# Performance work log

Hardware: AMD Instinct MI355X
Metric: run time of the kernel (lower is better)

## Reference

```python
import jax, jax.numpy as jnp
import numpy as np

N, E = 50000, 800000
IN_DIM, HID, HEADS, LAYERS = 128, 128, 4, 2
C = HID // HEADS  # per-head channels
LN_EPS = 1e-5


def _segment_softmax(logits, seg, num_segments):
    # logits: [E, H], seg: [E] target-node ids
    m = jax.ops.segment_max(logits, seg, num_segments=num_segments)  # [N, H]
    ex = jnp.exp(logits - m[seg])
    s = jax.ops.segment_sum(ex, seg, num_segments=num_segments)      # [N, H]
    return ex / s[seg]


def setup_inputs() -> dict:
    key = jax.random.key(0)
    ks = jax.random.split(key, 16)
    x = jax.random.normal(ks[0], (N, IN_DIM), dtype=jnp.float32)
    edge_index = jax.random.randint(ks[1], (2, E), 0, N, dtype=jnp.int64)
    edge_weight = jax.random.normal(ks[2], (E,), dtype=jnp.float32)
    s = 0.05
    # stacked per-layer params (in_ch == hidden for both layers since in_dim == hidden_dim)
    Wq = jax.random.normal(ks[3], (LAYERS, HID, HID), dtype=jnp.float32) * s
    bq = jnp.zeros((LAYERS, HID), dtype=jnp.float32)
    Wk = jax.random.normal(ks[4], (LAYERS, HID, HID), dtype=jnp.float32) * s
    bk = jnp.zeros((LAYERS, HID), dtype=jnp.float32)
    Wv = jax.random.normal(ks[5], (LAYERS, HID, HID), dtype=jnp.float32) * s
    bv = jnp.zeros((LAYERS, HID), dtype=jnp.float32)
    We = jax.random.normal(ks[6], (LAYERS, 1, HID), dtype=jnp.float32) * s  # lin_edge, no bias
    Wskip = jax.random.normal(ks[7], (LAYERS, HID, HID), dtype=jnp.float32) * s
    bskip = jnp.zeros((LAYERS, HID), dtype=jnp.float32)
    ln_g = jnp.ones((LAYERS, HID), dtype=jnp.float32)
    ln_b = jnp.zeros((LAYERS, HID), dtype=jnp.float32)
    return dict(x=x, edge_index=edge_index, edge_weight=edge_weight,
                Wq=Wq, bq=bq, Wk=Wk, bk=bk, Wv=Wv, bv=bv, We=We,
                Wskip=Wskip, bskip=bskip, ln_g=ln_g, ln_b=ln_b)


def reference(x, edge_index, edge_weight, Wq, bq, Wk, bk, Wv, bv, We, Wskip, bskip, ln_g, ln_b):
    # eval mode: dropout (on alpha and on features) is identity
    h = jnp.nan_to_num(x, nan=0.0, posinf=0.0, neginf=0.0)
    edge_attr = jnp.nan_to_num(edge_weight, nan=0.0, posinf=0.0, neginf=0.0)[:, None]  # [E,1]
    src, dst = edge_index[0], edge_index[1]  # PyG: x_j = x[src], softmax/aggregate over dst
    scale = 1.0 / jnp.sqrt(jnp.asarray(C, dtype=h.dtype))
    for l in range(LAYERS):
        h_res = h
        q = (h @ Wq[l] + bq[l]).reshape(N, HEADS, C)
        k = (h @ Wk[l] + bk[l]).reshape(N, HEADS, C)
        v = (h @ Wv[l] + bv[l]).reshape(N, HEADS, C)
        e = (edge_attr @ We[l]).reshape(E, HEADS, C)          # lin_edge (bias=False)
        kj = k[src] + e                                       # [E,H,C]
        logits = jnp.einsum('ehc,ehc->eh', q[dst], kj) * scale
        alpha = _segment_softmax(logits, dst, N)              # [E,H]
        msg = (v[src] + e) * alpha[..., None]                 # [E,H,C]
        out = jax.ops.segment_sum(msg, dst, num_segments=N).reshape(N, HID)
        out = out + h @ Wskip[l] + bskip[l]                   # root_weight skip (beta=False)
        out = jnp.nan_to_num(out, nan=0.0, posinf=0.0, neginf=0.0)
        mu = out.mean(axis=-1, keepdims=True)
        var = ((out - mu) ** 2).mean(axis=-1, keepdims=True)
        out = (out - mu) / jnp.sqrt(var + LN_EPS) * ln_g[l] + ln_b[l]
        out = jax.nn.relu(jnp.nan_to_num(out, nan=0.0, posinf=0.0, neginf=0.0))
        out = jnp.nan_to_num(out, nan=0.0, posinf=0.0, neginf=0.0)
        h = jnp.nan_to_num(out + h_res, nan=0.0, posinf=0.0, neginf=0.0)
    return h
```

## Files before the change

### kernel.cpp

```cpp
#include <hip/hip_runtime.h>
#include <hip/hip_fp16.h>
#include <math.h>

#define NN 50000
#define EE 800000
#define HID 128
#define LAYERS 2
#define LN_EPS 1e-5f
#define SCALE 0.17677669529663687f
#define NB 49

typedef _Float16 f16x8 __attribute__((ext_vector_type(8)));
typedef _Float16 h2 __attribute__((ext_vector_type(2)));
typedef float f32x4 __attribute__((ext_vector_type(4)));

__device__ __forceinline__ float sanitize(float f) {
    return (f == f && fabsf(f) != INFINITY) ? f : 0.0f;
}


__global__ void zero_deg_kernel(int* __restrict__ deg) {
    int i = blockIdx.x * blockDim.x + threadIdx.x;
    if (i < NN) deg[i] = 0;
}

__global__ void hist_kernel(const int* __restrict__ eidx, int* __restrict__ deg) {
    int e = blockIdx.x * blockDim.x + threadIdx.x;
    if (e < EE) atomicAdd(&deg[eidx[EE + e]], 1);
}


__global__ __launch_bounds__(1024) void deg_bsum_kernel(const int* __restrict__ deg,
                                                        int* __restrict__ bsum) {
    __shared__ int red[16];
    int tid = threadIdx.x;
    int i = blockIdx.x * 1024 + tid;
    int v = (i < NN) ? deg[i] : 0;
    #pragma unroll
    for (int off = 32; off >= 1; off >>= 1) v += __shfl_xor(v, off, 64);
    if ((tid & 63) == 0) red[tid >> 6] = v;
    __syncthreads();
    if (tid == 0) {
        int s = 0;
        #pragma unroll
        for (int w = 0; w < 16; ++w) s += red[w];
        bsum[blockIdx.x] = s;
    }
}

__global__ void bsum_scan_kernel(const int* __restrict__ bsum, int* __restrict__ boff,
                                 int* __restrict__ row_start) {
    int lane = threadIdx.x;
    int v = (lane < NB) ? bsum[lane] : 0;
    int sc = v;
    #pragma unroll
    for (int off = 1; off < 64; off <<= 1) {
        int t = __shfl_up(sc, off, 64);
        if (lane >= off) sc += t;
    }
    if (lane < NB) boff[lane] = sc - v;
    if (lane == 63) row_start[NN] = sc;
}

__global__ __launch_bounds__(1024) void deg_scan_kernel(const int* __restrict__ deg,
                                                        const int* __restrict__ boff,
                                                        int* __restrict__ row_start,
                                                        int* __restrict__ cursor) {
    __shared__ int wsum[16];
    int tid = threadIdx.x;
    int lane = tid & 63;
    int wid = tid >> 6;
    int i = blockIdx.x * 1024 + tid;
    int val = (i < NN) ? deg[i] : 0;
    int sc = val;
    #pragma unroll
    for (int off = 1; off < 64; off <<= 1) {
        int t = __shfl_up(sc, off, 64);
        if (lane >= off) sc += t;
    }
    if (lane == 63) wsum[wid] = sc;
    __syncthreads();
    if (wid == 0) {
        int s = (lane < 16) ? wsum[lane] : 0;
        #pragma unroll
        for (int off = 1; off < 16; off <<= 1) {
            int t = __shfl_up(s, off, 64);
            if (lane >= off) s += t;
        }
        if (lane < 16) wsum[lane] = s;
    }
    __syncthreads();
    int waveoff = (wid > 0) ? wsum[wid - 1] : 0;
    int excl = boff[blockIdx.x] + waveoff + sc - val;
    if (i < NN) {
        row_start[i] = excl;
        cursor[i] = excl;
    }
}

__global__ void scatter_kernel(const int* __restrict__ eidx,
                               const float* __restrict__ ew,
                               int* __restrict__ cursor,
                               long long* __restrict__ csr_pk) {
    int e = blockIdx.x * blockDim.x + threadIdx.x;
    if (e < EE) {
        int dst = eidx[EE + e];
        int src = eidx[e];
        int pos = atomicAdd(&cursor[dst], 1);
        unsigned wb = __float_as_uint(sanitize(ew[e]));
        csr_pk[pos] = ((long long)wb << 32) | (unsigned)src;
    }
}


__global__ void sanitize_kernel(const float* __restrict__ x, float* __restrict__ h0,
                                __half* __restrict__ hh) {
    int i = blockIdx.x * blockDim.x + threadIdx.x;
    if (i < NN * HID / 4) {
        float4 f = ((const float4*)x)[i];
        f.x = sanitize(f.x); f.y = sanitize(f.y); f.z = sanitize(f.z); f.w = sanitize(f.w);
        ((float4*)h0)[i] = f;
        __half2* hp = (__half2*)(hh + (size_t)i * 4);
        hp[0] = __floats2half2_rn(f.x, f.y);
        hp[1] = __floats2half2_rn(f.z, f.w);
    }
}


__global__ void wtcvt_kernel(const float* __restrict__ Wq, const float* __restrict__ Wk,
                             const float* __restrict__ Wv, const float* __restrict__ Wsk,
                             __half* __restrict__ WT) {
    int idx = blockIdx.x * blockDim.x + threadIdx.x;
    if (idx >= LAYERS * 4 * HID * HID) return;
    int k = idx & 127;
    int c = (idx >> 7) & 127;
    int m = (idx >> 14) & 3;
    int l = idx >> 16;
    const float* W = (m == 0) ? Wq : (m == 1) ? Wk : (m == 2) ? Wv : Wsk;
    WT[idx] = __float2half(W[l * HID * HID + k * HID + c]);
}


__global__ __launch_bounds__(256) void mfma_qkvs_kernel(
    const __half* __restrict__ hh, const __half* __restrict__ WT,
    const float* __restrict__ bq, const float* __restrict__ bk,
    const float* __restrict__ bv, const float* __restrict__ bsk,
    __half* __restrict__ qh, __half* __restrict__ kv, float* __restrict__ skf)
{
    int wid = threadIdx.x >> 6;
    int lane = threadIdx.x & 63;
    int row0 = blockIdx.x * 64 + wid * 16;
    int arow = row0 + (lane & 15);
    if (arow >= NN) arow = NN - 1;
    int ksub = (lane >> 4) * 8;

    const _Float16* hp = (const _Float16*)(hh + (size_t)arow * HID + ksub);
    f16x8 a0 = *(const f16x8*)(hp + 0);
    f16x8 a1 = *(const f16x8*)(hp + 32);
    f16x8 a2 = *(const f16x8*)(hp + 64);
    f16x8 a3 = *(const f16x8*)(hp + 96);

    #pragma unroll
    for (int m = 0; m < 4; ++m) {
        const _Float16* Wm = (const _Float16*)(WT + m * HID * HID);
        const float* bias = (m == 0) ? bq : (m == 1) ? bk : (m == 2) ? bv : bsk;
        #pragma unroll
        for (int t = 0; t < 8; ++t) {
            int col = t * 16 + (lane & 15);
            const _Float16* wc = Wm + (size_t)col * HID + ksub;
            f32x4 acc = {0.f, 0.f, 0.f, 0.f};
            acc = __builtin_amdgcn_mfma_f32_16x16x32_f16(a0, *(const f16x8*)(wc + 0),  acc, 0, 0, 0);
            acc = __builtin_amdgcn_mfma_f32_16x16x32_f16(a1, *(const f16x8*)(wc + 32), acc, 0, 0, 0);
            acc = __builtin_amdgcn_mfma_f32_16x16x32_f16(a2, *(const f16x8*)(wc + 64), acc, 0, 0, 0);
            acc = __builtin_amdgcn_mfma_f32_16x16x32_f16(a3, *(const f16x8*)(wc + 96), acc, 0, 0, 0);
            float bcol = bias[col];
            #pragma unroll
            for (int r = 0; r < 4; ++r) {
                int row = row0 + (lane >> 4) * 4 + r;
                if (row < NN) {
                    float val = acc[r] + bcol;
                    if (m == 0)      qh[(size_t)row * HID + col] = __float2half(val);
                    else if (m == 1) kv[(size_t)row * 256 + col] = __float2half(val);
                    else if (m == 2) kv[(size_t)row * 256 + 128 + col] = __float2half(val);
                    else             skf[(size_t)row * HID + col] = val;
                }
            }
        }
    }
}


struct OS8 { float m, s, tw; float a[8]; };

__device__ __forceinline__ void os8_init(OS8& o) {
    o.m = -INFINITY; o.s = 0.f; o.tw = 0.f;
    #pragma unroll
    for (int j = 0; j < 8; ++j) o.a[j] = 0.f;
}

__device__ __forceinline__ OS8 os8_mrg(OS8 a, OS8 b) {
    float mn = fmaxf(a.m, b.m);
    if (mn == -INFINITY) return a;
    float ca = __expf(a.m - mn);
    float cb = __expf(b.m - mn);
    OS8 r;
    r.m = mn;
    r.s  = a.s  * ca + b.s  * cb;
    r.tw = a.tw * ca + b.tw * cb;
    #pragma unroll
    for (int j = 0; j < 8; ++j) r.a[j] = a.a[j] * ca + b.a[j] * cb;
    return r;
}

__device__ __forceinline__ void edge_step(long long p, const __half* __restrict__ kv, int c0,
                                          h2 q01, h2 q23, h2 q45, h2 q67, float qwe, OS8& st) {
    int src = (int)(p & 0xffffffffLL);
    float w = __uint_as_float((unsigned)((unsigned long long)p >> 32));
    const _Float16* kvp = (const _Float16*)(kv + (size_t)src * 256);
    f16x8 k8 = *(const f16x8*)(kvp + c0);
    f16x8 v8 = *(const f16x8*)(kvp + 128 + c0);
    h2 k01 = {k8[0], k8[1]}, k23 = {k8[2], k8[3]}, k45 = {k8[4], k8[5]}, k67 = {k8[6], k8[7]};
    float d = __builtin_amdgcn_fdot2(k01, q01, 0.f, false);
    d = __builtin_amdgcn_fdot2(k23, q23, d, false);
    d = __builtin_amdgcn_fdot2(k45, q45, d, false);
    d = __builtin_amdgcn_fdot2(k67, q67, d, false);
    d += __shfl_xor(d, 1, 64);
    d += __shfl_xor(d, 2, 64);
    float l = fmaf(w, qwe, d) * SCALE;
    float mn = fmaxf(st.m, l);
    float cr = __expf(st.m - mn);
    float pp = __expf(l - mn);
    st.s  = fmaf(st.s,  cr, pp);
    st.tw = fmaf(st.tw, cr, pp * w);
    #pragma unroll
    for (int j = 0; j < 8; ++j) st.a[j] = fmaf(st.a[j], cr, pp * (float)v8[j]);
    st.m = mn;
}

__global__ __launch_bounds__(256) void agg_kernel(
    const __half* __restrict__ qh, const __half* __restrict__ kv,
    const float* __restrict__ skp, const float* __restrict__ hres,
    const float* __restrict__ We,
    const float* __restrict__ ln_g, const float* __restrict__ ln_b,
    const int* __restrict__ row_start, const long long* __restrict__ csr_pk,
    float* __restrict__ hout, __half* __restrict__ hh_out)
{
    int node = blockIdx.x * 16 + (threadIdx.x >> 4);
    int sl = threadIdx.x & 15;
    int c0 = sl * 8;

    f16x8 q8 = *(const f16x8*)((const _Float16*)qh + (size_t)node * HID + c0);
    h2 q01 = {q8[0], q8[1]}, q23 = {q8[2], q8[3]}, q45 = {q8[4], q8[5]}, q67 = {q8[6], q8[7]};

    float4 weA = *(const float4*)(We + c0);
    float4 weB = *(const float4*)(We + c0 + 4);
    float qwe = (float)q8[0] * weA.x + (float)q8[1] * weA.y + (float)q8[2] * weA.z + (float)q8[3] * weA.w
              + (float)q8[4] * weB.x + (float)q8[5] * weB.y + (float)q8[6] * weB.z + (float)q8[7] * weB.w;
    qwe += __shfl_xor(qwe, 1, 64);
    qwe += __shfl_xor(qwe, 2, 64);

    int rs = row_start[node];
    int re = row_start[node + 1];

    OS8 st0, st1, st2, st3;
    os8_init(st0); os8_init(st1); os8_init(st2); os8_init(st3);

    int i = rs;
    for (; i + 4 <= re; i += 4) {
        long long p0 = csr_pk[i + 0];
        long long p1 = csr_pk[i + 1];
        long long p2 = csr_pk[i + 2];
        long long p3 = csr_pk[i + 3];
        edge_step(p0, kv, c0, q01, q23, q45, q67, qwe, st0);
        edge_step(p1, kv, c0, q01, q23, q45, q67, qwe, st1);
        edge_step(p2, kv, c0, q01, q23, q45, q67, qwe, st2);
        edge_step(p3, kv, c0, q01, q23, q45, q67, qwe, st3);
    }
    for (; i < re; ++i) edge_step(csr_pk[i], kv, c0, q01, q23, q45, q67, qwe, st0);

    OS8 st = os8_mrg(os8_mrg(st0, st1), os8_mrg(st2, st3));

    float inv = (re > rs) ? 1.f / st.s : 0.f;
    float wef[8] = {weA.x, weA.y, weA.z, weA.w, weB.x, weB.y, weB.z, weB.w};

    float4 skA = *(const float4*)(skp + (size_t)node * HID + c0);
    float4 skB = *(const float4*)(skp + (size_t)node * HID + c0 + 4);
    float skv[8] = {skA.x, skA.y, skA.z, skA.w, skB.x, skB.y, skB.z, skB.w};

    float ox[8];
    float sum8 = 0.f;
    #pragma unroll
    for (int j = 0; j < 8; ++j) {
        float o = fmaf(st.tw, wef[j], st.a[j]) * inv;
        o = sanitize(o + skv[j]);
        ox[j] = o;
        sum8 += o;
    }

    float mu = sum8;
    mu += __shfl_xor(mu, 1, 64); mu += __shfl_xor(mu, 2, 64);
    mu += __shfl_xor(mu, 4, 64); mu += __shfl_xor(mu, 8, 64);
    mu *= (1.f / 128.f);

    float var8 = 0.f;
    #pragma unroll
    for (int j = 0; j < 8; ++j) {
        float dx = ox[j] - mu;
        var8 = fmaf(dx, dx, var8);
    }
    float var = var8;
    var += __shfl_xor(var, 1, 64); var += __shfl_xor(var, 2, 64);
    var += __shfl_xor(var, 4, 64); var += __shfl_xor(var, 8, 64);
    var *= (1.f / 128.f);
    float rstd = rsqrtf(var + LN_EPS);

    float4 gA = *(const float4*)(ln_g + c0);
    float4 gB = *(const float4*)(ln_g + c0 + 4);
    float4 bA = *(const float4*)(ln_b + c0);
    float4 bB = *(const float4*)(ln_b + c0 + 4);
    float gv[8] = {gA.x, gA.y, gA.z, gA.w, gB.x, gB.y, gB.z, gB.w};
    float bv_[8] = {bA.x, bA.y, bA.z, bA.w, bB.x, bB.y, bB.z, bB.w};

    float4 hrA = *(const float4*)(hres + (size_t)node * HID + c0);
    float4 hrB = *(const float4*)(hres + (size_t)node * HID + c0 + 4);
    float hr[8] = {hrA.x, hrA.y, hrA.z, hrA.w, hrB.x, hrB.y, hrB.z, hrB.w};

    float outv[8];
    _Float16 outh[8];
    #pragma unroll
    for (int j = 0; j < 8; ++j) {
        float rx = fmaxf(fmaf((ox[j] - mu) * rstd, gv[j], bv_[j]), 0.f);
        float o = sanitize(rx + hr[j]);
        outv[j] = o;
        outh[j] = (_Float16)o;
    }
    float* op = hout + (size_t)node * HID + c0;
    *(float4*)(op)     = make_float4(outv[0], outv[1], outv[2], outv[3]);
    *(float4*)(op + 4) = make_float4(outv[4], outv[5], outv[6], outv[7]);
    *(f16x8*)((_Float16*)hh_out + (size_t)node * HID + c0) =
        *(f16x8*)outh;
}


extern "C" void kernel_launch(void* const* d_in, const int* in_sizes, int n_in,
                              void* d_out, int out_size, void* d_ws, size_t ws_size,
                              hipStream_t stream) {
    const float* x      = (const float*)d_in[0];
    const int*   ei     = (const int*)d_in[1];
    const float* ew     = (const float*)d_in[2];
    const float* Wq     = (const float*)d_in[3];
    const float* bq     = (const float*)d_in[4];
    const float* Wk     = (const float*)d_in[5];
    const float* bk     = (const float*)d_in[6];
    const float* Wv     = (const float*)d_in[7];
    const float* bv     = (const float*)d_in[8];
    const float* We     = (const float*)d_in[9];
    const float* Wsk    = (const float*)d_in[10];
    const float* bsk    = (const float*)d_in[11];
    const float* ln_g   = (const float*)d_in[12];
    const float* ln_b   = (const float*)d_in[13];

    const size_t NH = (size_t)NN * HID;
    float* h0  = (float*)d_ws;
    float* h1  = h0 + NH;
    float* skf = h1 + NH;
    __half* hh = (__half*)(skf + NH);
    __half* qh = hh + NH;
    __half* kv = qh + NH;
    __half* WT = kv + 2 * NH;
    int* deg       = (int*)(WT + LAYERS * 4 * HID * HID);
    int* row_start = deg + NN;
    int* cursor    = row_start + NN + 2;
    int* bsum      = cursor + NN;
    int* boff      = bsum + 64;
    long long* csr_pk = (long long*)(boff + 64);

    zero_deg_kernel<<<(NN + 255) / 256, 256, 0, stream>>>(deg);
    hist_kernel<<<(EE + 255) / 256, 256, 0, stream>>>(ei, deg);
    deg_bsum_kernel<<<NB, 1024, 0, stream>>>(deg, bsum);
    bsum_scan_kernel<<<1, 64, 0, stream>>>(bsum, boff, row_start);
    deg_scan_kernel<<<NB, 1024, 0, stream>>>(deg, boff, row_start, cursor);
    scatter_kernel<<<(EE + 255) / 256, 256, 0, stream>>>(ei, ew, cursor, csr_pk);

    sanitize_kernel<<<(NN * HID / 4 + 255) / 256, 256, 0, stream>>>(x, h0, hh);
    wtcvt_kernel<<<(LAYERS * 4 * HID * HID + 255) / 256, 256, 0, stream>>>(Wq, Wk, Wv, Wsk, WT);

    const int WELEM = HID * HID;
    const int MROWS = (NN + 63) / 64;

    for (int l = 0; l < LAYERS; ++l) {
        const float* hin = (l == 0) ? h0 : h1;
        float* hout = (l == 0) ? h1 : (float*)d_out;
        mfma_qkvs_kernel<<<MROWS, 256, 0, stream>>>(
            hh, WT + (size_t)l * 4 * WELEM,
            bq + l * HID, bk + l * HID, bv + l * HID, bsk + l * HID,
            qh, kv, skf);
        agg_kernel<<<NN / 16, 256, 0, stream>>>(
            qh, kv, skf, hin,
            We + l * HID, ln_g + l * HID, ln_b + l * HID,
            row_start, csr_pk, hout, hh);
    }
}
```

Before: 472.8 us.

## Assign one wavefront per node and split edges across four lane groups

The aggregation kernel now maps each destination node to a full 64-lane wavefront instead of a 16-lane group. The four 16-lane groups each process an interleaved subset of the node's edges with two online-softmax states, then merge them through cross-group shuffles. The goal is more memory-level parallelism per node and shorter serial edge chains, since mean degree is 16. The cost is four times as many blocks, redundant epilogue work on three quarters of the lanes, and extra shuffle traffic for the merge.

```diff
diff --git a/kernel.cpp b/kernel.cpp
--- a/kernel.cpp
+++ b/kernel.cpp
@@ -212,6 +212,16 @@
     return r;
 }
 
+__device__ __forceinline__ OS8 os8_shfl_xor(const OS8& o, int mask) {
+    OS8 r;
+    r.m  = __shfl_xor(o.m,  mask, 64);
+    r.s  = __shfl_xor(o.s,  mask, 64);
+    r.tw = __shfl_xor(o.tw, mask, 64);
+    #pragma unroll
+    for (int j = 0; j < 8; ++j) r.a[j] = __shfl_xor(o.a[j], mask, 64);
+    return r;
+}
+
 __device__ __forceinline__ void edge_step(long long p, const __half* __restrict__ kv, int c0,
                                           h2 q01, h2 q23, h2 q45, h2 q67, float qwe, OS8& st) {
     int src = (int)(p & 0xffffffffLL);
@@ -245,8 +255,10 @@
     const int* __restrict__ row_start, const long long* __restrict__ csr_pk,
     float* __restrict__ hout, __half* __restrict__ hh_out)
 {
-    int node = blockIdx.x * 16 + (threadIdx.x >> 4);
-    int sl = threadIdx.x & 15;
+    int node = blockIdx.x * 4 + (threadIdx.x >> 6);
+    int lane = threadIdx.x & 63;
+    int grp = lane >> 4;
+    int sl = lane & 15;
     int c0 = sl * 8;
 
     f16x8 q8 = *(const f16x8*)((const _Float16*)qh + (size_t)node * HID + c0);
@@ -262,23 +274,21 @@
     int rs = row_start[node];
     int re = row_start[node + 1];
 
-    OS8 st0, st1, st2, st3;
-    os8_init(st0); os8_init(st1); os8_init(st2); os8_init(st3);
-
-    int i = rs;
-    for (; i + 4 <= re; i += 4) {
-        long long p0 = csr_pk[i + 0];
-        long long p1 = csr_pk[i + 1];
-        long long p2 = csr_pk[i + 2];
-        long long p3 = csr_pk[i + 3];
-        edge_step(p0, kv, c0, q01, q23, q45, q67, qwe, st0);
-        edge_step(p1, kv, c0, q01, q23, q45, q67, qwe, st1);
-        edge_step(p2, kv, c0, q01, q23, q45, q67, qwe, st2);
-        edge_step(p3, kv, c0, q01, q23, q45, q67, qwe, st3);
-    }
-    for (; i < re; ++i) edge_step(csr_pk[i], kv, c0, q01, q23, q45, q67, qwe, st0);
-
-    OS8 st = os8_mrg(os8_mrg(st0, st1), os8_mrg(st2, st3));
+    OS8 s0, s1;
+    os8_init(s0); os8_init(s1);
+
+    int i = rs + grp;
+    for (; i + 4 < re; i += 8) {
+        long long p0 = csr_pk[i];
+        long long p1 = csr_pk[i + 4];
+        edge_step(p0, kv, c0, q01, q23, q45, q67, qwe, s0);
+        edge_step(p1, kv, c0, q01, q23, q45, q67, qwe, s1);
+    }
+    if (i < re) edge_step(csr_pk[i], kv, c0, q01, q23, q45, q67, qwe, s0);
+
+    OS8 st = os8_mrg(s0, s1);
+    st = os8_mrg(st, os8_shfl_xor(st, 16));
+    st = os8_mrg(st, os8_shfl_xor(st, 32));
 
     float inv = (re > rs) ? 1.f / st.s : 0.f;
     float wef[8] = {weA.x, weA.y, weA.z, weA.w, weB.x, weB.y, weB.z, weB.w};
@@ -314,31 +324,32 @@
     var *= (1.f / 128.f);
     float rstd = rsqrtf(var + LN_EPS);
 
-    float4 gA = *(const float4*)(ln_g + c0);
-    float4 gB = *(const float4*)(ln_g + c0 + 4);
-    float4 bA = *(const float4*)(ln_b + c0);
-    float4 bB = *(const float4*)(ln_b + c0 + 4);
-    float gv[8] = {gA.x, gA.y, gA.z, gA.w, gB.x, gB.y, gB.z, gB.w};
-    float bv_[8] = {bA.x, bA.y, bA.z, bA.w, bB.x, bB.y, bB.z, bB.w};
-
-    float4 hrA = *(const float4*)(hres + (size_t)node * HID + c0);
-    float4 hrB = *(const float4*)(hres + (size_t)node * HID + c0 + 4);
-    float hr[8] = {hrA.x, hrA.y, hrA.z, hrA.w, hrB.x, hrB.y, hrB.z, hrB.w};
-
-    float outv[8];
-    _Float16 outh[8];
-    #pragma unroll
-    for (int j = 0; j < 8; ++j) {
-        float rx = fmaxf(fmaf((ox[j] - mu) * rstd, gv[j], bv_[j]), 0.f);
-        float o = sanitize(rx + hr[j]);
-        outv[j] = o;
-        outh[j] = (_Float16)o;
-    }
-    float* op = hout + (size_t)node * HID + c0;
-    *(float4*)(op)     = make_float4(outv[0], outv[1], outv[2], outv[3]);
-    *(float4*)(op + 4) = make_float4(outv[4], outv[5], outv[6], outv[7]);
-    *(f16x8*)((_Float16*)hh_out + (size_t)node * HID + c0) =
-        *(f16x8*)outh;
+    if (grp == 0) {
+        float4 gA = *(const float4*)(ln_g + c0);
+        float4 gB = *(const float4*)(ln_g + c0 + 4);
+        float4 bA = *(const float4*)(ln_b + c0);
+        float4 bB = *(const float4*)(ln_b + c0 + 4);
+        float gv[8] = {gA.x, gA.y, gA.z, gA.w, gB.x, gB.y, gB.z, gB.w};
+        float bv_[8] = {bA.x, bA.y, bA.z, bA.w, bB.x, bB.y, bB.z, bB.w};
+
+        float4 hrA = *(const float4*)(hres + (size_t)node * HID + c0);
+        float4 hrB = *(const float4*)(hres + (size_t)node * HID + c0 + 4);
+        float hr[8] = {hrA.x, hrA.y, hrA.z, hrA.w, hrB.x, hrB.y, hrB.z, hrB.w};
+
+        float outv[8];
+        _Float16 outh[8];
+        #pragma unroll
+        for (int j = 0; j < 8; ++j) {
+            float rx = fmaxf(fmaf((ox[j] - mu) * rstd, gv[j], bv_[j]), 0.f);
+            float o = sanitize(rx + hr[j]);
+            outv[j] = o;
+            outh[j] = (_Float16)o;
+        }
+        float* op = hout + (size_t)node * HID + c0;
+        *(float4*)(op)     = make_float4(outv[0], outv[1], outv[2], outv[3]);
+        *(float4*)(op + 4) = make_float4(outv[4], outv[5], outv[6], outv[7]);
+        *(f16x8*)((_Float16*)hh_out + (size_t)node * HID + c0) = *(f16x8*)outh;
+    }
 }
 
 
@@ -395,7 +406,7 @@
             hh, WT + (size_t)l * 4 * WELEM,
             bq + l * HID, bk + l * HID, bv + l * HID, bsk + l * HID,
             qh, kv, skf);
-        agg_kernel<<<NN / 16, 256, 0, stream>>>(
+        agg_kernel<<<NN / 4, 256, 0, stream>>>(
             qh, kv, skf, hin,
             We + l * HID, ln_g + l * HID, ln_b + l * HID,
             row_start, csr_pk, hout, hh);
```

Result: no change. 469.7 us (-0.7%).
